# Kernel optimization log

Hardware: AMD Instinct MI355X
Metric: run time of the kernel (lower is better)

Reference implementation:

```python
import jax, jax.numpy as jnp
import numpy as np

N_NODES = 100000
N_EDGES = 1600000
F_IN = 256
F_HID = 128
BN_EPS = 1e-3


def setup_inputs() -> dict:
    key = jax.random.key(0)
    ks = jax.random.split(key, 10)
    x = jax.random.normal(ks[0], (N_NODES, F_IN), dtype=jnp.float32)
    edge_index = jax.random.randint(ks[1], (2, N_EDGES), 0, N_NODES, dtype=jnp.int64)
    edge_weight = jax.random.uniform(ks[2], (N_EDGES,), dtype=jnp.float32)
    # Layer 0: GCNConv 256 -> 128, Layer 1: GCNConv 128 -> 128
    W0 = jax.random.normal(ks[3], (F_IN, F_HID), dtype=jnp.float32) * (1.0 / np.sqrt(F_IN))
    b0 = jnp.zeros((F_HID,), dtype=jnp.float32)
    g0 = jnp.ones((F_HID,), dtype=jnp.float32)
    beta0 = jnp.zeros((F_HID,), dtype=jnp.float32)
    W1 = jax.random.normal(ks[4], (F_HID, F_HID), dtype=jnp.float32) * (1.0 / np.sqrt(F_HID))
    b1 = jnp.zeros((F_HID,), dtype=jnp.float32)
    g1 = jnp.ones((F_HID,), dtype=jnp.float32)
    beta1 = jnp.zeros((F_HID,), dtype=jnp.float32)
    return {"x": x, "edge_index": edge_index, "edge_weight": edge_weight,
            "W0": W0, "b0": b0, "g0": g0, "beta0": beta0,
            "W1": W1, "b1": b1, "g1": g1, "beta1": beta1}


def _gcn_conv(x, src, dst, ew, W, b):
    # PyG GCNConv: add self-loops (weight 1), symmetric normalization,
    # linear transform, scatter-aggregate over destination, then bias.
    h = x @ W                                            # [N, F_out]
    deg = jax.ops.segment_sum(ew, dst, num_segments=N_NODES) + 1.0  # +1 self-loop
    dinv = jnp.where(deg > 0, jax.lax.rsqrt(deg), 0.0)   # deg^{-1/2}
    norm = dinv[src] * ew * dinv[dst]                    # [E]
    agg = jax.ops.segment_sum(h[src] * norm[:, None], dst, num_segments=N_NODES)
    agg = agg + (dinv * dinv)[:, None] * h               # self-loop contribution
    return agg + b


def _batchnorm(x, gamma, beta):
    # training-mode BatchNorm1d math (batch stats, biased variance), eps=1e-3
    mu = jnp.mean(x, axis=0)
    var = jnp.mean(jnp.square(x - mu), axis=0)
    return (x - mu) * jax.lax.rsqrt(var + BN_EPS) * gamma + beta


def reference(x, edge_index, edge_weight, W0, b0, g0, beta0, W1, b1, g1, beta1):
    src, dst = edge_index[0], edge_index[1]
    # Layer 0: GCNConv -> BatchNorm -> ReLU -> Dropout(eval=identity)
    h = _gcn_conv(x, src, dst, edge_weight, W0, b0)
    h = jax.nn.relu(_batchnorm(h, g0, beta0))
    # Layer 1
    h = _gcn_conv(h, src, dst, edge_weight, W1, b1)
    h = jax.nn.relu(_batchnorm(h, g1, beta1))
    return h
```

## Files before the change

### kernel.cpp

```cpp
#include <hip/hip_runtime.h>
#include <stdint.h>

#define FIN 256
#define FHID 128
#define BN_EPS 1e-3f

typedef short bf16x8 __attribute__((ext_vector_type(8)));
typedef float f32x4 __attribute__((ext_vector_type(4)));

__device__ inline short f2bf(float f) {
    unsigned u = __float_as_uint(f);
    unsigned r = (u + 0x7FFFu + ((u >> 16) & 1u)) >> 16;
    return (short)r;
}
__device__ inline float bflo(unsigned v) { return __uint_as_float(v << 16); }
__device__ inline float bfhi(unsigned v) { return __uint_as_float(v & 0xFFFF0000u); }
__device__ inline float bf2f(short s) {
    return __uint_as_float(((unsigned)(unsigned short)s) << 16);
}

#define DEG_SCALE 131072.0f
#define DEG_INV   (1.0f / 131072.0f)

__global__ __launch_bounds__(256) void k_histprep(const int* __restrict__ ei, int E,
                                                  int CB, int CHUNK, int nbuk,
                                                  unsigned* __restrict__ bcnt,
                                                  const float* __restrict__ W0,
                                                  const float* __restrict__ W1,
                                                  short* __restrict__ Wt0,
                                                  short* __restrict__ Wt1) {
    __shared__ unsigned hist[1024];
    if ((int)blockIdx.x < CB) {
        for (int i = threadIdx.x; i < nbuk; i += 256) hist[i] = 0;
        __syncthreads();
        const int e0 = blockIdx.x * CHUNK;
        const int e1 = min(e0 + CHUNK, E);
        for (int e = e0 + threadIdx.x; e < e1; e += 256)
            atomicAdd(&hist[ei[E + e] >> 7], 1u);
        __syncthreads();
        for (int k = threadIdx.x; k < nbuk; k += 256)
            bcnt[(size_t)blockIdx.x * nbuk + k] = hist[k];
    } else {
        int idx = ((int)blockIdx.x - CB) * 256 + threadIdx.x;
        if (idx < 32768) {
            int n = idx >> 8, k = idx & 255;
            Wt0[idx] = f2bf(W0[k * 128 + n]);
        } else {
            int j = idx - 32768;
            if (j < 16384) {
                int n = j >> 7, k = j & 127;
                Wt1[j] = f2bf(W1[k * 128 + n]);
            }
        }
    }
}

__global__ __launch_bounds__(256, 2) void k_gemm0(const float* __restrict__ X,
                                                  const short* __restrict__ Wt,
                                                  short* __restrict__ H, int nrows) {
    const int lane = threadIdx.x & 63;
    const int w = threadIdx.x >> 6;
    const int r0 = blockIdx.x * 32;
    const int n0 = w * 32;
    const int l15 = lane & 15;
    const int lk = (lane >> 4) * 8;

    int row0 = r0 + l15;        if (row0 >= nrows) row0 = nrows - 1;
    int row1 = r0 + 16 + l15;   if (row1 >= nrows) row1 = nrows - 1;
    const float* rp[2] = { X + (size_t)row0 * 256 + lk, X + (size_t)row1 * 256 + lk };

    f32x4 acc[2][2];
#pragma unroll
    for (int mf = 0; mf < 2; mf++)
#pragma unroll
        for (int nf = 0; nf < 2; nf++)
#pragma unroll
            for (int r = 0; r < 4; r++) acc[mf][nf][r] = 0.0f;

#pragma unroll
    for (int ch = 0; ch < 2; ch++) {
        float4 u[4][2][2];
#pragma unroll
        for (int mf = 0; mf < 2; mf++)
#pragma unroll
            for (int c = 0; c < 4; c++) {
                u[c][mf][0] = *reinterpret_cast<const float4*>(rp[mf] + (ch * 4 + c) * 32);
                u[c][mf][1] = *reinterpret_cast<const float4*>(rp[mf] + (ch * 4 + c) * 32 + 4);
            }
#pragma unroll
        for (int c = 0; c < 4; c++) {
            const int ks = ch * 4 + c;
            bf16x8 a[2];
#pragma unroll
            for (int mf = 0; mf < 2; mf++) {
                const float4 u0 = u[c][mf][0], u1 = u[c][mf][1];
                bf16x8 t;
                t[0] = f2bf(u0.x); t[1] = f2bf(u0.y); t[2] = f2bf(u0.z); t[3] = f2bf(u0.w);
                t[4] = f2bf(u1.x); t[5] = f2bf(u1.y); t[6] = f2bf(u1.z); t[7] = f2bf(u1.w);
                a[mf] = t;
            }
            const bf16x8 b0 = *reinterpret_cast<const bf16x8*>(
                Wt + (size_t)(n0 + l15) * 256 + ks * 32 + lk);
            const bf16x8 b1 = *reinterpret_cast<const bf16x8*>(
                Wt + (size_t)(n0 + 16 + l15) * 256 + ks * 32 + lk);
            acc[0][0] = __builtin_amdgcn_mfma_f32_16x16x32_bf16(a[0], b0, acc[0][0], 0, 0, 0);
            acc[1][0] = __builtin_amdgcn_mfma_f32_16x16x32_bf16(a[1], b0, acc[1][0], 0, 0, 0);
            acc[0][1] = __builtin_amdgcn_mfma_f32_16x16x32_bf16(a[0], b1, acc[0][1], 0, 0, 0);
            acc[1][1] = __builtin_amdgcn_mfma_f32_16x16x32_bf16(a[1], b1, acc[1][1], 0, 0, 0);
        }
    }

#pragma unroll
    for (int mf = 0; mf < 2; mf++) {
        const int rbase = r0 + mf * 16 + (lane >> 4) * 4;
#pragma unroll
        for (int r = 0; r < 4; r++) {
            const int row = rbase + r;
            if (row < nrows) {
#pragma unroll
                for (int nf = 0; nf < 2; nf++)
                    H[(size_t)row * 128 + n0 + nf * 16 + l15] = f2bf(acc[mf][nf][r]);
            }
        }
    }
}

__global__ __launch_bounds__(256, 2) void k_gemm1(const short* __restrict__ X,
                                                  const short* __restrict__ Wt,
                                                  const float* __restrict__ prm,
                                                  short* __restrict__ H, int nrows) {
    const int lane = threadIdx.x & 63;
    const int w = threadIdx.x >> 6;
    const int r0 = blockIdx.x * 32;
    const int n0 = w * 32;
    const int l15 = lane & 15;
    const int lk = (lane >> 4) * 8;

    bf16x8 araw[4][2];
#pragma unroll
    for (int mf = 0; mf < 2; mf++) {
        int row = r0 + mf * 16 + l15;
        if (row >= nrows) row = nrows - 1;
        const short* rp = X + (size_t)row * 128 + lk;
#pragma unroll
        for (int ks = 0; ks < 4; ks++)
            araw[ks][mf] = *reinterpret_cast<const bf16x8*>(rp + ks * 32);
    }

    f32x4 acc[2][2];
#pragma unroll
    for (int mf = 0; mf < 2; mf++)
#pragma unroll
        for (int nf = 0; nf < 2; nf++)
#pragma unroll
            for (int r = 0; r < 4; r++) acc[mf][nf][r] = 0.0f;

#pragma unroll
    for (int ks = 0; ks < 4; ks++) {
        const int kb = ks * 32 + lk;
        const float4 sc0 = *reinterpret_cast<const float4*>(prm + kb);
        const float4 sc1 = *reinterpret_cast<const float4*>(prm + kb + 4);
        const float4 sh0 = *reinterpret_cast<const float4*>(prm + 128 + kb);
        const float4 sh1 = *reinterpret_cast<const float4*>(prm + 128 + kb + 4);
        bf16x8 a[2];
#pragma unroll
        for (int mf = 0; mf < 2; mf++) {
            const bf16x8 ar = araw[ks][mf];
            bf16x8 t;
            t[0] = f2bf(fmaxf(bf2f(ar[0]) * sc0.x + sh0.x, 0.f));
            t[1] = f2bf(fmaxf(bf2f(ar[1]) * sc0.y + sh0.y, 0.f));
            t[2] = f2bf(fmaxf(bf2f(ar[2]) * sc0.z + sh0.z, 0.f));
            t[3] = f2bf(fmaxf(bf2f(ar[3]) * sc0.w + sh0.w, 0.f));
            t[4] = f2bf(fmaxf(bf2f(ar[4]) * sc1.x + sh1.x, 0.f));
            t[5] = f2bf(fmaxf(bf2f(ar[5]) * sc1.y + sh1.y, 0.f));
            t[6] = f2bf(fmaxf(bf2f(ar[6]) * sc1.z + sh1.z, 0.f));
            t[7] = f2bf(fmaxf(bf2f(ar[7]) * sc1.w + sh1.w, 0.f));
            a[mf] = t;
        }
        const bf16x8 b0 = *reinterpret_cast<const bf16x8*>(
            Wt + (size_t)(n0 + l15) * 128 + kb);
        const bf16x8 b1 = *reinterpret_cast<const bf16x8*>(
            Wt + (size_t)(n0 + 16 + l15) * 128 + kb);
        acc[0][0] = __builtin_amdgcn_mfma_f32_16x16x32_bf16(a[0], b0, acc[0][0], 0, 0, 0);
        acc[1][0] = __builtin_amdgcn_mfma_f32_16x16x32_bf16(a[1], b0, acc[1][0], 0, 0, 0);
        acc[0][1] = __builtin_amdgcn_mfma_f32_16x16x32_bf16(a[0], b1, acc[0][1], 0, 0, 0);
        acc[1][1] = __builtin_amdgcn_mfma_f32_16x16x32_bf16(a[1], b1, acc[1][1], 0, 0, 0);
    }

#pragma unroll
    for (int mf = 0; mf < 2; mf++) {
        const int rbase = r0 + mf * 16 + (lane >> 4) * 4;
#pragma unroll
        for (int r = 0; r < 4; r++) {
            const int row = rbase + r;
            if (row < nrows) {
#pragma unroll
                for (int nf = 0; nf < 2; nf++)
                    H[(size_t)row * 128 + n0 + nf * 16 + l15] = f2bf(acc[mf][nf][r]);
            }
        }
    }
}

__global__ __launch_bounds__(256) void k_phaseB(unsigned* __restrict__ bcnt,
                                                unsigned* __restrict__ btotal,
                                                int CB, int nbuk) {
    __shared__ unsigned lds[256];
    const int k = blockIdx.x;
    const int t = threadIdx.x;
    unsigned v = (t < CB) ? bcnt[(size_t)t * nbuk + k] : 0;
    lds[t] = v;
    __syncthreads();
    for (int off = 1; off < 256; off <<= 1) {
        unsigned add = (t >= off) ? lds[t - off] : 0;
        __syncthreads();
        lds[t] += add;
        __syncthreads();
    }
    if (t < CB) bcnt[(size_t)t * nbuk + k] = lds[t] - v;
    if (t == 255) btotal[k] = lds[255];
}

__global__ __launch_bounds__(256) void k_bsum(const unsigned* __restrict__ btotal,
                                              unsigned* __restrict__ bbase,
                                              int nbuk, int E) {
    __shared__ unsigned lds[256];
    const int t = threadIdx.x;
    unsigned v[4];
    unsigned s = 0;
#pragma unroll
    for (int i = 0; i < 4; i++) {
        int j = t * 4 + i;
        v[i] = (j < nbuk) ? btotal[j] : 0;
        s += v[i];
    }
    lds[t] = s;
    __syncthreads();
    for (int off = 1; off < 256; off <<= 1) {
        unsigned add = (t >= off) ? lds[t - off] : 0;
        __syncthreads();
        lds[t] += add;
        __syncthreads();
    }
    unsigned run = lds[t] - s;
#pragma unroll
    for (int i = 0; i < 4; i++) {
        int j = t * 4 + i;
        if (j < nbuk) bbase[j] = run;
        run += v[i];
    }
    if (t == 255) bbase[nbuk] = (unsigned)E;
}

__global__ __launch_bounds__(256) void k_phaseC(const int* __restrict__ ei,
                                                const float* __restrict__ ew,
                                                int E, int CB, int CHUNK, int nbuk,
                                                const unsigned* __restrict__ bcur,
                                                const unsigned* __restrict__ bbase,
                                                int2* __restrict__ recs_mid) {
    __shared__ unsigned curs[1024];
    const int b = blockIdx.x;
    for (int k = threadIdx.x; k < nbuk; k += 256)
        curs[k] = bbase[k] + bcur[(size_t)b * nbuk + k];
    __syncthreads();
    const int e0 = b * CHUNK;
    const int e1 = min(e0 + CHUNK, E);
    for (int e = e0 + threadIdx.x; e < e1; e += 256) {
        int src = ei[e];
        int dst = ei[E + e];
        unsigned pos = atomicAdd(&curs[dst >> 7], 1u);
        recs_mid[pos] = make_int2(src | ((dst & 127) << 17), __float_as_int(ew[e]));
    }
}

__global__ __launch_bounds__(256) void k_phaseD(const int2* __restrict__ recs_mid,
                                                const unsigned* __restrict__ bbase,
                                                float* __restrict__ dinv,
                                                int* __restrict__ rowptr,
                                                int2* __restrict__ recs,
                                                int n, int E) {
    __shared__ unsigned cnt[128], wsum[128], rank[128], sc[128], base[128];
    __shared__ float dloc[128];
    const int k = blockIdx.x;
    const int t = threadIdx.x;
    if (t < 128) { cnt[t] = 0; wsum[t] = 0; rank[t] = 0; }
    __syncthreads();
    const unsigned s0 = bbase[k], s1 = bbase[k + 1];
    for (unsigned i = s0 + t; i < s1; i += 256) {
        int2 r = recs_mid[i];
        int dl = (r.x >> 17) & 127;
        atomicAdd(&cnt[dl], 1u);
        atomicAdd(&wsum[dl], (unsigned)(__int_as_float(r.y) * DEG_SCALE));
    }
    __syncthreads();
    if (t < 128) sc[t] = cnt[t];
    __syncthreads();
    for (int off = 1; off < 128; off <<= 1) {
        unsigned add = (t < 128 && t >= off) ? sc[t - off] : 0;
        __syncthreads();
        if (t < 128) sc[t] += add;
        __syncthreads();
    }
    if (t < 128) {
        unsigned excl = sc[t] - cnt[t];
        base[t] = s0 + excl;
        int dst = k * 128 + t;
        if (dst < n) {
            float deg = (float)wsum[t] * DEG_INV + 1.0f;
            float dv = rsqrtf(deg);
            dloc[t] = dv;
            dinv[dst] = dv;
            rowptr[dst] = (int)(s0 + excl);
        }
    }
    if (k == 0 && t == 0) rowptr[n] = E;
    __syncthreads();
    for (unsigned i = s0 + t; i < s1; i += 256) {
        int2 r = recs_mid[i];
        int dl = (r.x >> 17) & 127;
        unsigned rr = atomicAdd(&rank[dl], 1u);
        float w2 = __int_as_float(r.y) * dloc[dl];
        recs[base[dl] + rr] = make_int2(r.x & 0x1FFFF, __float_as_int(w2));
    }
}

__global__ __launch_bounds__(256) void k_phaseE(int2* __restrict__ recs,
                                                const float* __restrict__ dinv, int E) {
    int i = blockIdx.x * 256 + threadIdx.x;
    if (i < E) {
        int2 r = recs[i];
        float w = __int_as_float(r.y) * dinv[r.x];
        recs[i] = make_int2(r.x, __float_as_int(w));
    }
}

__global__ __launch_bounds__(256) void k_gather_stats(const short* __restrict__ h,
                                                      short* __restrict__ aggbf,
                                                      const int* __restrict__ rowptr,
                                                      const int2* __restrict__ recs,
                                                      const float* __restrict__ dinv,
                                                      const float* __restrict__ bias,
                                                      float* __restrict__ partial,
                                                      int n, int nstreams) {
    __shared__ float lsum[4][128], lsq[4][128];
    const int w = threadIdx.x >> 6;
    const int lane = threadIdx.x & 63;
    const int q3 = lane >> 4;
    const int f8 = (lane & 15) * 8;
    const float4 bv0 = *reinterpret_cast<const float4*>(bias + f8);
    const float4 bv1 = *reinterpret_cast<const float4*>(bias + f8 + 4);
    float s[8], qq[8];
#pragma unroll
    for (int j = 0; j < 8; j++) { s[j] = 0.f; qq[j] = 0.f; }

    for (int node = blockIdx.x * 16 + w * 4 + q3; node < n; node += nstreams) {
        float a[8];
#pragma unroll
        for (int j = 0; j < 8; j++) a[j] = 0.f;
        int e = rowptr[node];
        const int end = rowptr[node + 1];
        for (; e + 4 <= end; e += 4) {
            const int2 r0 = recs[e];
            const int2 r1 = recs[e + 1];
            const int2 r2 = recs[e + 2];
            const int2 r3 = recs[e + 3];
            const uint4 v0 = *reinterpret_cast<const uint4*>(h + (size_t)r0.x * 128 + f8);
            const uint4 v1 = *reinterpret_cast<const uint4*>(h + (size_t)r1.x * 128 + f8);
            const uint4 v2 = *reinterpret_cast<const uint4*>(h + (size_t)r2.x * 128 + f8);
            const uint4 v3 = *reinterpret_cast<const uint4*>(h + (size_t)r3.x * 128 + f8);
            const float w0 = __int_as_float(r0.y);
            const float w1 = __int_as_float(r1.y);
            const float w2 = __int_as_float(r2.y);
            const float w3 = __int_as_float(r3.y);
            a[0] += bflo(v0.x) * w0; a[1] += bfhi(v0.x) * w0;
            a[2] += bflo(v0.y) * w0; a[3] += bfhi(v0.y) * w0;
            a[4] += bflo(v0.z) * w0; a[5] += bfhi(v0.z) * w0;
            a[6] += bflo(v0.w) * w0; a[7] += bfhi(v0.w) * w0;
            a[0] += bflo(v1.x) * w1; a[1] += bfhi(v1.x) * w1;
            a[2] += bflo(v1.y) * w1; a[3] += bfhi(v1.y) * w1;
            a[4] += bflo(v1.z) * w1; a[5] += bfhi(v1.z) * w1;
            a[6] += bflo(v1.w) * w1; a[7] += bfhi(v1.w) * w1;
            a[0] += bflo(v2.x) * w2; a[1] += bfhi(v2.x) * w2;
            a[2] += bflo(v2.y) * w2; a[3] += bfhi(v2.y) * w2;
            a[4] += bflo(v2.z) * w2; a[5] += bfhi(v2.z) * w2;
            a[6] += bflo(v2.w) * w2; a[7] += bfhi(v2.w) * w2;
            a[0] += bflo(v3.x) * w3; a[1] += bfhi(v3.x) * w3;
            a[2] += bflo(v3.y) * w3; a[3] += bfhi(v3.y) * w3;
            a[4] += bflo(v3.z) * w3; a[5] += bfhi(v3.z) * w3;
            a[6] += bflo(v3.w) * w3; a[7] += bfhi(v3.w) * w3;
        }
        for (; e < end; e++) {
            const int2 r = recs[e];
            const uint4 v = *reinterpret_cast<const uint4*>(h + (size_t)r.x * 128 + f8);
            const float w0 = __int_as_float(r.y);
            a[0] += bflo(v.x) * w0; a[1] += bfhi(v.x) * w0;
            a[2] += bflo(v.y) * w0; a[3] += bfhi(v.y) * w0;
            a[4] += bflo(v.z) * w0; a[5] += bfhi(v.z) * w0;
            a[6] += bflo(v.w) * w0; a[7] += bfhi(v.w) * w0;
        }
        const float di = dinv[node];
        const float sl = di * di;
        const uint4 hv = *reinterpret_cast<const uint4*>(h + (size_t)node * 128 + f8);
        float o[8];
        o[0] = a[0] + bflo(hv.x) * sl + bv0.x;
        o[1] = a[1] + bfhi(hv.x) * sl + bv0.y;
        o[2] = a[2] + bflo(hv.y) * sl + bv0.z;
        o[3] = a[3] + bfhi(hv.y) * sl + bv0.w;
        o[4] = a[4] + bflo(hv.z) * sl + bv1.x;
        o[5] = a[5] + bfhi(hv.z) * sl + bv1.y;
        o[6] = a[6] + bflo(hv.w) * sl + bv1.z;
        o[7] = a[7] + bfhi(hv.w) * sl + bv1.w;
        bf16x8 ob;
#pragma unroll
        for (int j = 0; j < 8; j++) ob[j] = f2bf(o[j]);
        *reinterpret_cast<bf16x8*>(aggbf + (size_t)node * 128 + f8) = ob;
#pragma unroll
        for (int j = 0; j < 8; j++) { s[j] += o[j]; qq[j] += o[j] * o[j]; }
    }

#pragma unroll
    for (int j = 0; j < 8; j++) {
        s[j] += __shfl_xor(s[j], 16);  s[j] += __shfl_xor(s[j], 32);
        qq[j] += __shfl_xor(qq[j], 16); qq[j] += __shfl_xor(qq[j], 32);
    }
    if (q3 == 0) {
        *reinterpret_cast<float4*>(&lsum[w][f8]) = make_float4(s[0], s[1], s[2], s[3]);
        *reinterpret_cast<float4*>(&lsum[w][f8 + 4]) = make_float4(s[4], s[5], s[6], s[7]);
        *reinterpret_cast<float4*>(&lsq[w][f8]) = make_float4(qq[0], qq[1], qq[2], qq[3]);
        *reinterpret_cast<float4*>(&lsq[w][f8 + 4]) = make_float4(qq[4], qq[5], qq[6], qq[7]);
    }
    __syncthreads();
    const int t = threadIdx.x;
    if (t < 128) {
        float ps = lsum[0][t] + lsum[1][t] + lsum[2][t] + lsum[3][t];
        float pq = lsq[0][t] + lsq[1][t] + lsq[2][t] + lsq[3][t];
        partial[(size_t)blockIdx.x * 256 + t] = ps;
        partial[(size_t)blockIdx.x * 256 + 128 + t] = pq;
    }
}

__global__ __launch_bounds__(256) void k_stats_bn(const float* __restrict__ partial,
                                                  const float* __restrict__ g,
                                                  const float* __restrict__ beta,
                                                  float* __restrict__ prm,
                                                  int nblk, int n) {
    __shared__ float wsm[4], wqm[4];
    const int f = blockIdx.x;
    const int t = threadIdx.x;
    const int per = nblk / 256;
    float s = 0.f, q = 0.f;
    for (int i = 0; i < per; i++) {
        int p = t * per + i;
        s += partial[(size_t)p * 256 + f];
        q += partial[(size_t)p * 256 + 128 + f];
    }
#pragma unroll
    for (int off = 1; off < 64; off <<= 1) {
        s += __shfl_xor(s, off);
        q += __shfl_xor(q, off);
    }
    if ((t & 63) == 0) { wsm[t >> 6] = s; wqm[t >> 6] = q; }
    __syncthreads();
    if (t == 0) {
        float S = wsm[0] + wsm[1] + wsm[2] + wsm[3];
        float Q = wqm[0] + wqm[1] + wqm[2] + wqm[3];
        float inv_n = 1.0f / (float)n;
        float mu = S * inv_n;
        float var = Q * inv_n - mu * mu;
        float sc = rsqrtf(var + BN_EPS) * g[f];
        prm[f] = sc;
        prm[128 + f] = beta[f] - mu * sc;
    }
}

__global__ __launch_bounds__(256) void k_bn_relu(const short* __restrict__ xbf,
                                                 float* __restrict__ y,
                                                 const float* __restrict__ prm, int n) {
    int idx = blockIdx.x * blockDim.x + threadIdx.x;
    const int total = n * 16;
    for (; idx < total; idx += gridDim.x * blockDim.x) {
        int node = idx >> 4;
        int f8 = (idx & 15) * 8;
        const uint4 v = *reinterpret_cast<const uint4*>(xbf + (size_t)node * 128 + f8);
        const float4 sc0 = *reinterpret_cast<const float4*>(prm + f8);
        const float4 sc1 = *reinterpret_cast<const float4*>(prm + f8 + 4);
        const float4 sh0 = *reinterpret_cast<const float4*>(prm + 128 + f8);
        const float4 sh1 = *reinterpret_cast<const float4*>(prm + 128 + f8 + 4);
        float4 o0, o1;
        o0.x = fmaxf(bflo(v.x) * sc0.x + sh0.x, 0.f);
        o0.y = fmaxf(bfhi(v.x) * sc0.y + sh0.y, 0.f);
        o0.z = fmaxf(bflo(v.y) * sc0.z + sh0.z, 0.f);
        o0.w = fmaxf(bfhi(v.y) * sc0.w + sh0.w, 0.f);
        o1.x = fmaxf(bflo(v.z) * sc1.x + sh1.x, 0.f);
        o1.y = fmaxf(bfhi(v.z) * sc1.y + sh1.y, 0.f);
        o1.z = fmaxf(bflo(v.w) * sc1.z + sh1.z, 0.f);
        o1.w = fmaxf(bfhi(v.w) * sc1.w + sh1.w, 0.f);
        float* yp = y + (size_t)node * 128 + f8;
        *reinterpret_cast<float4*>(yp) = o0;
        *reinterpret_cast<float4*>(yp + 4) = o1;
    }
}

extern "C" void kernel_launch(void* const* d_in, const int* in_sizes, int n_in,
                              void* d_out, int out_size, void* d_ws, size_t ws_size,
                              hipStream_t stream) {
    const float* x   = (const float*)d_in[0];
    const int*   ei  = (const int*)d_in[1];
    const float* ew  = (const float*)d_in[2];
    const float* W0  = (const float*)d_in[3];
    const float* b0  = (const float*)d_in[4];
    const float* g0  = (const float*)d_in[5];
    const float* be0 = (const float*)d_in[6];
    const float* W1  = (const float*)d_in[7];
    const float* b1  = (const float*)d_in[8];
    const float* g1  = (const float*)d_in[9];
    const float* be1 = (const float*)d_in[10];
    float* out = (float*)d_out;

    const int N = in_sizes[0] / FIN;
    const int E = in_sizes[2];
    const int NBUK = (N + 127) >> 7;
    const int CB = 256;
    const int CHUNK = (E + CB - 1) / CB;
    const int GB = 2048;

    short* aggbf    = (short*)d_ws;
    short* hbf      = aggbf + (size_t)N * 128;
    int2*  recs     = (int2*)(hbf + (size_t)N * 128);
    int2*  recs_mid = recs + E;
    unsigned* bcnt  = (unsigned*)(recs_mid + E);
    unsigned* btotal= bcnt + (size_t)CB * NBUK;
    unsigned* bbase = btotal + NBUK;
    float* dinv     = (float*)(bbase + NBUK + 1);
    int*   rowptr   = (int*)(dinv + N);
    float* prm      = (float*)(rowptr + N + 1);
    float* partial  = prm + 256;

    short* Wt0 = (short*)d_out;
    short* Wt1 = Wt0 + 256 * 128;

    const int gemm_blocks = (N + 31) / 32;

    k_histprep<<<CB + 192, 256, 0, stream>>>(ei, E, CB, CHUNK, NBUK, bcnt,
                                             W0, W1, Wt0, Wt1);
    k_gemm0<<<gemm_blocks, 256, 0, stream>>>(x, Wt0, hbf, N);

    k_phaseB<<<NBUK, 256, 0, stream>>>(bcnt, btotal, CB, NBUK);
    k_bsum<<<1, 256, 0, stream>>>(btotal, bbase, NBUK, E);
    k_phaseC<<<CB, 256, 0, stream>>>(ei, ew, E, CB, CHUNK, NBUK, bcnt, bbase, recs_mid);
    k_phaseD<<<NBUK, 256, 0, stream>>>(recs_mid, bbase, dinv, rowptr, recs, N, E);
    k_phaseE<<<(E + 255) / 256, 256, 0, stream>>>(recs, dinv, E);

    k_gather_stats<<<GB, 256, 0, stream>>>(hbf, aggbf, rowptr, recs, dinv, b0,
                                           partial, N, GB * 16);
    k_stats_bn<<<128, 256, 0, stream>>>(partial, g0, be0, prm, GB, N);

    k_gemm1<<<gemm_blocks, 256, 0, stream>>>(aggbf, Wt1, prm, hbf, N);
    k_gather_stats<<<GB, 256, 0, stream>>>(hbf, aggbf, rowptr, recs, dinv, b1,
                                           partial, N, GB * 16);
    k_stats_bn<<<128, 256, 0, stream>>>(partial, g1, be1, prm, GB, N);
    k_bn_relu<<<2048, 256, 0, stream>>>(aggbf, out, prm, N);
}
```

Measured before the change: 353.1 us.

## Stage GEMM input rows through swizzled LDS and widen histogram pass to more blocks

Both GEMM kernels now first stage their 32-row input tile into shared memory, using direct global-to-LDS loads when the builtin is available and an XOR swizzle to avoid bank conflicts. Each wave then reads its A fragments from LDS instead of issuing strided per-lane global loads. Separately, the edge histogram is spread over 1024 blocks instead of 256, and the prefix-scan kernel folds four sub-histograms per thread so the scatter pass can keep its 256 chunks. This adds LDS use per block, drops the occupancy hint on the GEMMs, and produces a larger bcnt buffer.

Result: faster. 321.7 us (-8.9%).

```diff
diff --git a/kernel.cpp b/kernel.cpp
--- a/kernel.cpp
+++ b/kernel.cpp
@@ -4,6 +4,18 @@
 #define FIN 256
 #define FHID 128
 #define BN_EPS 1e-3f
+
+#ifndef USE_GLL
+#if defined(__has_builtin)
+#if __has_builtin(__builtin_amdgcn_global_load_lds)
+#define USE_GLL 1
+#else
+#define USE_GLL 0
+#endif
+#else
+#define USE_GLL 0
+#endif
+#endif
 
 typedef short bf16x8 __attribute__((ext_vector_type(8)));
 typedef float f32x4 __attribute__((ext_vector_type(4)));
@@ -23,25 +35,25 @@
 #define DEG_INV   (1.0f / 131072.0f)
 
 __global__ __launch_bounds__(256) void k_histprep(const int* __restrict__ ei, int E,
-                                                  int CB, int CHUNK, int nbuk,
+                                                  int HB, int CHUNKH, int nbuk,
                                                   unsigned* __restrict__ bcnt,
                                                   const float* __restrict__ W0,
                                                   const float* __restrict__ W1,
                                                   short* __restrict__ Wt0,
                                                   short* __restrict__ Wt1) {
     __shared__ unsigned hist[1024];
-    if ((int)blockIdx.x < CB) {
+    if ((int)blockIdx.x < HB) {
         for (int i = threadIdx.x; i < nbuk; i += 256) hist[i] = 0;
         __syncthreads();
-        const int e0 = blockIdx.x * CHUNK;
-        const int e1 = min(e0 + CHUNK, E);
+        const int e0 = blockIdx.x * CHUNKH;
+        const int e1 = min(e0 + CHUNKH, E);
         for (int e = e0 + threadIdx.x; e < e1; e += 256)
             atomicAdd(&hist[ei[E + e] >> 7], 1u);
         __syncthreads();
         for (int k = threadIdx.x; k < nbuk; k += 256)
             bcnt[(size_t)blockIdx.x * nbuk + k] = hist[k];
     } else {
-        int idx = ((int)blockIdx.x - CB) * 256 + threadIdx.x;
+        int idx = ((int)blockIdx.x - HB) * 256 + threadIdx.x;
         if (idx < 32768) {
             int n = idx >> 8, k = idx & 255;
             Wt0[idx] = f2bf(W0[k * 128 + n]);
@@ -55,19 +67,35 @@
     }
 }
 
-__global__ __launch_bounds__(256, 2) void k_gemm0(const float* __restrict__ X,
-                                                  const short* __restrict__ Wt,
-                                                  short* __restrict__ H, int nrows) {
-    const int lane = threadIdx.x & 63;
-    const int w = threadIdx.x >> 6;
+__global__ __launch_bounds__(256) void k_gemm0(const float* __restrict__ X,
+                                               const short* __restrict__ Wt,
+                                               short* __restrict__ H, int nrows) {
+    __shared__ float xs[8192];
+    const int t = threadIdx.x;
+    const int lane = t & 63;
+    const int w = t >> 6;
     const int r0 = blockIdx.x * 32;
+    const int l15 = lane & 15;
+    const int q = lane >> 4;
+
+#pragma unroll
+    for (int i = 0; i < 8; i++) {
+        const int row = w * 8 + i;
+        int grow = r0 + row; if (grow >= nrows) grow = nrows - 1;
+        const char* gsrc = (const char*)(X + (size_t)grow * 256);
+        const int swz = (row & 7) << 4;
+#if USE_GLL
+        __builtin_amdgcn_global_load_lds(gsrc + ((lane * 16) ^ swz),
+                                         xs + row * 256, 16, 0, 0);
+#else
+        const float4 v = *reinterpret_cast<const float4*>(gsrc + ((lane * 16) ^ swz));
+        *reinterpret_cast<float4*>((char*)xs + row * 1024 + lane * 16) = v;
+#endif
+    }
+    __syncthreads();
+
     const int n0 = w * 32;
-    const int l15 = lane & 15;
-    const int lk = (lane >> 4) * 8;
-
-    int row0 = r0 + l15;        if (row0 >= nrows) row0 = nrows - 1;
-    int row1 = r0 + 16 + l15;   if (row1 >= nrows) row1 = nrows - 1;
-    const float* rp[2] = { X + (size_t)row0 * 256 + lk, X + (size_t)row1 * 256 + lk };
+    const int swzr = (l15 & 7) << 4;
 
     f32x4 acc[2][2];
 #pragma unroll
@@ -78,36 +106,27 @@
             for (int r = 0; r < 4; r++) acc[mf][nf][r] = 0.0f;
 
 #pragma unroll
-    for (int ch = 0; ch < 2; ch++) {
-        float4 u[4][2][2];
-#pragma unroll
-        for (int mf = 0; mf < 2; mf++)
-#pragma unroll
-            for (int c = 0; c < 4; c++) {
-                u[c][mf][0] = *reinterpret_cast<const float4*>(rp[mf] + (ch * 4 + c) * 32);
-                u[c][mf][1] = *reinterpret_cast<const float4*>(rp[mf] + (ch * 4 + c) * 32 + 4);
-            }
-#pragma unroll
-        for (int c = 0; c < 4; c++) {
-            const int ks = ch * 4 + c;
-            bf16x8 a[2];
-#pragma unroll
-            for (int mf = 0; mf < 2; mf++) {
-                const float4 u0 = u[c][mf][0], u1 = u[c][mf][1];
-                bf16x8 t;
-                t[0] = f2bf(u0.x); t[1] = f2bf(u0.y); t[2] = f2bf(u0.z); t[3] = f2bf(u0.w);
-                t[4] = f2bf(u1.x); t[5] = f2bf(u1.y); t[6] = f2bf(u1.z); t[7] = f2bf(u1.w);
-                a[mf] = t;
-            }
-            const bf16x8 b0 = *reinterpret_cast<const bf16x8*>(
-                Wt + (size_t)(n0 + l15) * 256 + ks * 32 + lk);
-            const bf16x8 b1 = *reinterpret_cast<const bf16x8*>(
-                Wt + (size_t)(n0 + 16 + l15) * 256 + ks * 32 + lk);
-            acc[0][0] = __builtin_amdgcn_mfma_f32_16x16x32_bf16(a[0], b0, acc[0][0], 0, 0, 0);
-            acc[1][0] = __builtin_amdgcn_mfma_f32_16x16x32_bf16(a[1], b0, acc[1][0], 0, 0, 0);
-            acc[0][1] = __builtin_amdgcn_mfma_f32_16x16x32_bf16(a[0], b1, acc[0][1], 0, 0, 0);
-            acc[1][1] = __builtin_amdgcn_mfma_f32_16x16x32_bf16(a[1], b1, acc[1][1], 0, 0, 0);
-        }
+    for (int ks = 0; ks < 8; ks++) {
+        const int cb = ks * 128 + q * 32;
+        bf16x8 a[2];
+#pragma unroll
+        for (int mf = 0; mf < 2; mf++) {
+            const char* rb = (const char*)xs + (size_t)(mf * 16 + l15) * 1024;
+            const float4 u0 = *reinterpret_cast<const float4*>(rb + (cb ^ swzr));
+            const float4 u1 = *reinterpret_cast<const float4*>(rb + ((cb + 16) ^ swzr));
+            bf16x8 tt;
+            tt[0] = f2bf(u0.x); tt[1] = f2bf(u0.y); tt[2] = f2bf(u0.z); tt[3] = f2bf(u0.w);
+            tt[4] = f2bf(u1.x); tt[5] = f2bf(u1.y); tt[6] = f2bf(u1.z); tt[7] = f2bf(u1.w);
+            a[mf] = tt;
+        }
+        const bf16x8 b0 = *reinterpret_cast<const bf16x8*>(
+            Wt + (size_t)(n0 + l15) * 256 + ks * 32 + q * 8);
+        const bf16x8 b1 = *reinterpret_cast<const bf16x8*>(
+            Wt + (size_t)(n0 + 16 + l15) * 256 + ks * 32 + q * 8);
+        acc[0][0] = __builtin_amdgcn_mfma_f32_16x16x32_bf16(a[0], b0, acc[0][0], 0, 0, 0);
+        acc[1][0] = __builtin_amdgcn_mfma_f32_16x16x32_bf16(a[1], b0, acc[1][0], 0, 0, 0);
+        acc[0][1] = __builtin_amdgcn_mfma_f32_16x16x32_bf16(a[0], b1, acc[0][1], 0, 0, 0);
+        acc[1][1] = __builtin_amdgcn_mfma_f32_16x16x32_bf16(a[1], b1, acc[1][1], 0, 0, 0);
     }
 
 #pragma unroll
@@ -125,27 +144,37 @@
     }
 }
 
-__global__ __launch_bounds__(256, 2) void k_gemm1(const short* __restrict__ X,
-                                                  const short* __restrict__ Wt,
-                                                  const float* __restrict__ prm,
-                                                  short* __restrict__ H, int nrows) {
-    const int lane = threadIdx.x & 63;
-    const int w = threadIdx.x >> 6;
+__global__ __launch_bounds__(256) void k_gemm1(const short* __restrict__ X,
+                                               const short* __restrict__ Wt,
+                                               const float* __restrict__ prm,
+                                               short* __restrict__ H, int nrows) {
+    __shared__ short xs[4096];
+    const int t = threadIdx.x;
+    const int lane = t & 63;
+    const int w = t >> 6;
     const int r0 = blockIdx.x * 32;
+    const int l15 = lane & 15;
+    const int q = lane >> 4;
+
+#pragma unroll
+    for (int j = 0; j < 2; j++) {
+        const int rbase = w * 8 + j * 4;
+        const int row = rbase + q;
+        int grow = r0 + row; if (grow >= nrows) grow = nrows - 1;
+        const char* gsrc = (const char*)(X + (size_t)grow * 128);
+        const int swz = (row & 7) << 4;
+#if USE_GLL
+        __builtin_amdgcn_global_load_lds(gsrc + (((lane & 15) * 16) ^ swz),
+                                         xs + rbase * 128, 16, 0, 0);
+#else
+        const uint4 v = *reinterpret_cast<const uint4*>(gsrc + (((lane & 15) * 16) ^ swz));
+        *reinterpret_cast<uint4*>((char*)xs + rbase * 256 + lane * 16) = v;
+#endif
+    }
+    __syncthreads();
+
     const int n0 = w * 32;
-    const int l15 = lane & 15;
-    const int lk = (lane >> 4) * 8;
-
-    bf16x8 araw[4][2];
-#pragma unroll
-    for (int mf = 0; mf < 2; mf++) {
-        int row = r0 + mf * 16 + l15;
-        if (row >= nrows) row = nrows - 1;
-        const short* rp = X + (size_t)row * 128 + lk;
-#pragma unroll
-        for (int ks = 0; ks < 4; ks++)
-            araw[ks][mf] = *reinterpret_cast<const bf16x8*>(rp + ks * 32);
-    }
+    const int swzr = (l15 & 7) << 4;
 
     f32x4 acc[2][2];
 #pragma unroll
@@ -157,7 +186,8 @@
 
 #pragma unroll
     for (int ks = 0; ks < 4; ks++) {
-        const int kb = ks * 32 + lk;
+        const int kb = ks * 32 + q * 8;
+        const int cb = ks * 64 + q * 16;
         const float4 sc0 = *reinterpret_cast<const float4*>(prm + kb);
         const float4 sc1 = *reinterpret_cast<const float4*>(prm + kb + 4);
         const float4 sh0 = *reinterpret_cast<const float4*>(prm + 128 + kb);
@@ -165,17 +195,18 @@
         bf16x8 a[2];
 #pragma unroll
         for (int mf = 0; mf < 2; mf++) {
-            const bf16x8 ar = araw[ks][mf];
-            bf16x8 t;
-            t[0] = f2bf(fmaxf(bf2f(ar[0]) * sc0.x + sh0.x, 0.f));
-            t[1] = f2bf(fmaxf(bf2f(ar[1]) * sc0.y + sh0.y, 0.f));
-            t[2] = f2bf(fmaxf(bf2f(ar[2]) * sc0.z + sh0.z, 0.f));
-            t[3] = f2bf(fmaxf(bf2f(ar[3]) * sc0.w + sh0.w, 0.f));
-            t[4] = f2bf(fmaxf(bf2f(ar[4]) * sc1.x + sh1.x, 0.f));
-            t[5] = f2bf(fmaxf(bf2f(ar[5]) * sc1.y + sh1.y, 0.f));
-            t[6] = f2bf(fmaxf(bf2f(ar[6]) * sc1.z + sh1.z, 0.f));
-            t[7] = f2bf(fmaxf(bf2f(ar[7]) * sc1.w + sh1.w, 0.f));
-            a[mf] = t;
+            const char* rb = (const char*)xs + (size_t)(mf * 16 + l15) * 256;
+            const bf16x8 ar = *reinterpret_cast<const bf16x8*>(rb + (cb ^ swzr));
+            bf16x8 tt;
+            tt[0] = f2bf(fmaxf(bf2f(ar[0]) * sc0.x + sh0.x, 0.f));
+            tt[1] = f2bf(fmaxf(bf2f(ar[1]) * sc0.y + sh0.y, 0.f));
+            tt[2] = f2bf(fmaxf(bf2f(ar[2]) * sc0.z + sh0.z, 0.f));
+            tt[3] = f2bf(fmaxf(bf2f(ar[3]) * sc0.w + sh0.w, 0.f));
+            tt[4] = f2bf(fmaxf(bf2f(ar[4]) * sc1.x + sh1.x, 0.f));
+            tt[5] = f2bf(fmaxf(bf2f(ar[5]) * sc1.y + sh1.y, 0.f));
+            tt[6] = f2bf(fmaxf(bf2f(ar[6]) * sc1.z + sh1.z, 0.f));
+            tt[7] = f2bf(fmaxf(bf2f(ar[7]) * sc1.w + sh1.w, 0.f));
+            a[mf] = tt;
         }
         const bf16x8 b0 = *reinterpret_cast<const bf16x8*>(
             Wt + (size_t)(n0 + l15) * 128 + kb);
@@ -204,12 +235,19 @@
 
 __global__ __launch_bounds__(256) void k_phaseB(unsigned* __restrict__ bcnt,
                                                 unsigned* __restrict__ btotal,
-                                                int CB, int nbuk) {
+                                                int HB, int nbuk) {
     __shared__ unsigned lds[256];
     const int k = blockIdx.x;
     const int t = threadIdx.x;
-    unsigned v = (t < CB) ? bcnt[(size_t)t * nbuk + k] : 0;
-    lds[t] = v;
+    unsigned v[4];
+    unsigned s = 0;
+#pragma unroll
+    for (int i = 0; i < 4; i++) {
+        int j = t * 4 + i;
+        v[i] = (j < HB) ? bcnt[(size_t)j * nbuk + k] : 0;
+        s += v[i];
+    }
+    lds[t] = s;
     __syncthreads();
     for (int off = 1; off < 256; off <<= 1) {
         unsigned add = (t >= off) ? lds[t - off] : 0;
@@ -217,7 +255,13 @@
         lds[t] += add;
         __syncthreads();
     }
-    if (t < CB) bcnt[(size_t)t * nbuk + k] = lds[t] - v;
+    unsigned run = lds[t] - s;
+#pragma unroll
+    for (int i = 0; i < 4; i++) {
+        int j = t * 4 + i;
+        if (j < HB) bcnt[(size_t)j * nbuk + k] = run;
+        run += v[i];
+    }
     if (t == 255) btotal[k] = lds[255];
 }
 
@@ -254,17 +298,17 @@
 
 __global__ __launch_bounds__(256) void k_phaseC(const int* __restrict__ ei,
                                                 const float* __restrict__ ew,
-                                                int E, int CB, int CHUNK, int nbuk,
-                                                const unsigned* __restrict__ bcur,
+                                                int E, int CHUNKC, int nbuk, int sub,
+                                                const unsigned* __restrict__ bcnt,
                                                 const unsigned* __restrict__ bbase,
                                                 int2* __restrict__ recs_mid) {
     __shared__ unsigned curs[1024];
     const int b = blockIdx.x;
     for (int k = threadIdx.x; k < nbuk; k += 256)
-        curs[k] = bbase[k] + bcur[(size_t)b * nbuk + k];
-    __syncthreads();
-    const int e0 = b * CHUNK;
-    const int e1 = min(e0 + CHUNK, E);
+        curs[k] = bbase[k] + bcnt[(size_t)(b * sub) * nbuk + k];
+    __syncthreads();
+    const int e0 = b * CHUNKC;
+    const int e1 = min(e0 + CHUNKC, E);
     for (int e = e0 + threadIdx.x; e < e1; e += 256) {
         int src = ei[e];
         int dst = ei[E + e];
@@ -520,8 +564,11 @@
     const int N = in_sizes[0] / FIN;
     const int E = in_sizes[2];
     const int NBUK = (N + 127) >> 7;
-    const int CB = 256;
-    const int CHUNK = (E + CB - 1) / CB;
+    const int HB = 1024;
+    const int CHUNKH = (E + HB - 1) / HB;
+    const int CBC = 256;
+    const int SUB = HB / CBC;
+    const int CHUNKC = CHUNKH * SUB;
     const int GB = 2048;
 
     short* aggbf    = (short*)d_ws;
@@ -529,7 +576,7 @@
     int2*  recs     = (int2*)(hbf + (size_t)N * 128);
     int2*  recs_mid = recs + E;
     unsigned* bcnt  = (unsigned*)(recs_mid + E);
-    unsigned* btotal= bcnt + (size_t)CB * NBUK;
+    unsigned* btotal= bcnt + (size_t)HB * NBUK;
     unsigned* bbase = btotal + NBUK;
     float* dinv     = (float*)(bbase + NBUK + 1);
     int*   rowptr   = (int*)(dinv + N);
@@ -541,13 +588,13 @@
 
     const int gemm_blocks = (N + 31) / 32;
 
-    k_histprep<<<CB + 192, 256, 0, stream>>>(ei, E, CB, CHUNK, NBUK, bcnt,
+    k_histprep<<<HB + 192, 256, 0, stream>>>(ei, E, HB, CHUNKH, NBUK, bcnt,
                                              W0, W1, Wt0, Wt1);
     k_gemm0<<<gemm_blocks, 256, 0, stream>>>(x, Wt0, hbf, N);
 
-    k_phaseB<<<NBUK, 256, 0, stream>>>(bcnt, btotal, CB, NBUK);
+    k_phaseB<<<NBUK, 256, 0, stream>>>(bcnt, btotal, HB, NBUK);
     k_bsum<<<1, 256, 0, stream>>>(btotal, bbase, NBUK, E);
-    k_phaseC<<<CB, 256, 0, stream>>>(ei, ew, E, CB, CHUNK, NBUK, bcnt, bbase, recs_mid);
+    k_phaseC<<<CBC, 256, 0, stream>>>(ei, ew, E, CHUNKC, NBUK, SUB, bcnt, bbase, recs_mid);
     k_phaseD<<<NBUK, 256, 0, stream>>>(recs_mid, bbase, dinv, rowptr, recs, N, E);
     k_phaseE<<<(E + 255) / 256, 256, 0, stream>>>(recs, dinv, E);
 
```
